# Kernel optimization log

Measured on AMD Instinct MI355X. Metric: run time of the kernel, lower is better.

## Reference

```python
import jax, jax.numpy as jnp
import numpy as np

B, C_IN, C_OUT, A, H, W = 32, 256, 512, 256, 64, 64


def setup_inputs() -> dict:
    key = jax.random.key(0)
    ks = jax.random.split(key, 8)
    s = 0.02
    return {
        "x": jax.random.normal(ks[0], (B, C_IN, H, W), dtype=jnp.float32),
        "g": jax.random.normal(ks[1], (B, C_OUT), dtype=jnp.float32),
        "Wg": jax.random.normal(ks[2], (A, C_OUT), dtype=jnp.float32) * s,
        "bg": jnp.full((A,), 0.1, dtype=jnp.float32),
        "Wx": jax.random.normal(ks[3], (A, C_IN), dtype=jnp.float32) * s,
        "bx": jnp.full((A,), 0.1, dtype=jnp.float32),
        "Wf": jax.random.normal(ks[4], (1, A), dtype=jnp.float32) * s,
        "bf": jnp.full((1,), 0.1, dtype=jnp.float32),
    }


def reference(x, g, Wg, bg, Wx, bx, Wf, bf):
    b, c, h, w = x.shape
    gg = g @ Wg.T + bg                                  # [B, A]
    xf = x.reshape(b, c, h * w)                          # [B, C, HW]
    # Linear_x applied per spatial position (batched instead of python loop)
    nx = jnp.einsum('bcn,ac->bna', xf, Wx) + bx          # [B, HW, A]
    nx = jax.nn.relu(gg[:, None, :] + nx)                # [B, HW, A]
    att = jnp.einsum('bna,a->bn', nx, Wf[0]) + bf[0]     # [B, HW]
    # min-subtract, sum-divide normalization
    att = att - jnp.min(att, axis=1, keepdims=True)
    att = att / jnp.sum(att, axis=1, keepdims=True)
    out = jnp.einsum('bcn,bn->bc', xf, att)              # weighted pooling [B, C]
    return out, att.reshape(b, h, w)
```

## Files before the change

### kernel.cpp

```cpp
#include <hip/hip_runtime.h>
#include <stdint.h>

#define B_   32
#define CIN  256
#define COUT 512
#define HW_  4096
#define NT   64

typedef short  short8  __attribute__((ext_vector_type(8)));
typedef float  float4_ __attribute__((ext_vector_type(4)));

__device__ __forceinline__ unsigned f2bf(float f) {
    unsigned u = __float_as_uint(f);
    u += 0x7FFFu + ((u >> 16) & 1u);
    return u >> 16;
}

__global__ __launch_bounds__(256) void prep_kernel(
    const float* __restrict__ g, const float* __restrict__ Wg,
    const float* __restrict__ bg, const float* __restrict__ Wx,
    const float* __restrict__ bx,
    uint4* __restrict__ WxR, float* __restrict__ ggbx,
    float* __restrict__ P, float* __restrict__ T)
{
    int t = threadIdx.x;
    if (blockIdx.x >= 32) {
        int e = (blockIdx.x - 32) * 256 + t;
        int lane = e & 63, ai = (e >> 6) & 3, kk = (e >> 8) & 7, w = e >> 11;
        int a  = w * 64 + ai * 16 + (lane & 15);
        int kb = kk * 32 + (lane >> 4) * 8;
        const float4* s = (const float4*)(Wx + (size_t)a * 256 + kb);
        float4 u0 = s[0], u1 = s[1];
        uint4 pk;
        pk.x = f2bf(u0.x) | (f2bf(u0.y) << 16);
        pk.y = f2bf(u0.z) | (f2bf(u0.w) << 16);
        pk.z = f2bf(u1.x) | (f2bf(u1.y) << 16);
        pk.w = f2bf(u1.z) | (f2bf(u1.w) << 16);
        WxR[e] = pk;
        return;
    }
    int b = blockIdx.x;
    int i = b * 256 + t;
    P[i] = 0.f; T[i] = 0.f;

    __shared__ float gl[COUT];
    gl[t]       = g[b * COUT + t];
    gl[t + 256] = g[b * COUT + 256 + t];
    __syncthreads();

    float acc0 = bg[t] + bx[t], acc1 = 0.f;
    const float4* wr = (const float4*)(Wg + (size_t)t * COUT);
    #pragma unroll 8
    for (int co = 0; co < COUT / 4; co += 2) {
        float4 wv0 = wr[co],     gv0 = *(const float4*)&gl[co * 4];
        float4 wv1 = wr[co + 1], gv1 = *(const float4*)&gl[co * 4 + 4];
        acc0 += wv0.x * gv0.x + wv0.y * gv0.y + wv0.z * gv0.z + wv0.w * gv0.w;
        acc1 += wv1.x * gv1.x + wv1.y * gv1.y + wv1.z * gv1.z + wv1.w * gv1.w;
    }
    ggbx[b * 256 + t] = acc0 + acc1;
}

__global__ __launch_bounds__(256, 2) void attn_main(
    const float* __restrict__ x, const char* __restrict__ WxR,
    const float* __restrict__ ggbx, const float* __restrict__ Wf,
    const float* __restrict__ bfs,
    float* __restrict__ P, float* __restrict__ T, float* __restrict__ raw)
{
    __shared__ float xTf[CIN * NT];
    __shared__ float att_part[4][NT];
    __shared__ float raw_l[NT];

    int bid = blockIdx.x;
    int b = bid >> 6, nt = bid & 63;
    int t = threadIdx.x, w = t >> 6, lane = t & 63;
    int quad = lane >> 4, l15 = lane & 15;

    const float* xb = x + (size_t)b * CIN * HW_ + nt * NT;

    {
        const float* gl0 = xb + (size_t)(lane >> 4) * HW_ + (lane & 15) * 4;
        #pragma unroll
        for (int j = 0; j < 16; j++) {
            int c0 = w * 64 + j * 4;
            __builtin_amdgcn_global_load_lds(
                (const __attribute__((address_space(1))) unsigned int*)(gl0 + (size_t)c0 * HW_),
                (__attribute__((address_space(3))) unsigned int*)&xTf[c0 * 64],
                16, 0, 0);
        }
    }

    float ga[4], wfv[4];
    #pragma unroll
    for (int ai = 0; ai < 4; ai++) {
        int a = w * 64 + ai * 16 + l15;
        ga[ai]  = ggbx[b * 256 + a];
        wfv[ai] = Wf[a];
    }

    float4_ acc[4][4];
    #pragma unroll
    for (int mi = 0; mi < 4; mi++)
        #pragma unroll
        for (int ai = 0; ai < 4; ai++)
            acc[mi][ai] = (float4_){0.f, 0.f, 0.f, 0.f};

    __syncthreads();

    const char* wsl = WxR + w * 32768 + lane * 16;
    short8 afA[4], bfA[4], afB[4], bfB[4];

    auto LDB = [&](short8* bf, int k0) {
        const char* wk = wsl + (k0 >> 5) * 4096;
        #pragma unroll
        for (int ai = 0; ai < 4; ai++)
            bf[ai] = *(const short8*)(wk + ai * 1024);
    };
    auto LDA = [&](short8* af, int k0) {
        int cb = k0 + quad * 8;
        #pragma unroll
        for (int mi = 0; mi < 4; mi++) {
            const float* bse = &xTf[cb * 64 + mi * 16 + l15];
            union { unsigned u[4]; short8 s; } cv;
            #pragma unroll
            for (int p = 0; p < 4; p++) {
                float f0 = bse[(2 * p) * 64];
                float f1 = bse[(2 * p + 1) * 64];
                cv.u[p] = f2bf(f0) | (f2bf(f1) << 16);
            }
            af[mi] = cv.s;
        }
    };
    auto MM = [&](short8* af, short8* bf) {
        #pragma unroll
        for (int mi = 0; mi < 4; mi++)
            #pragma unroll
            for (int ai = 0; ai < 4; ai++)
                acc[mi][ai] = __builtin_amdgcn_mfma_f32_16x16x32_bf16(
                    af[mi], bf[ai], acc[mi][ai], 0, 0, 0);
    };

    LDA(afA, 0);   LDB(bfA, 0);
    LDA(afB, 32);  LDB(bfB, 32);
    MM(afA, bfA);  LDA(afA, 64);  LDB(bfA, 64);
    MM(afB, bfB);  LDA(afB, 96);  LDB(bfB, 96);
    MM(afA, bfA);  LDA(afA, 128); LDB(bfA, 128);
    MM(afB, bfB);  LDA(afB, 160); LDB(bfB, 160);
    MM(afA, bfA);  LDA(afA, 192); LDB(bfA, 192);
    MM(afB, bfB);  LDA(afB, 224); LDB(bfB, 224);
    MM(afA, bfA);
    MM(afB, bfB);

    #pragma unroll
    for (int mi = 0; mi < 4; mi++) {
        float p[4] = {0.f, 0.f, 0.f, 0.f};
        #pragma unroll
        for (int ai = 0; ai < 4; ai++) {
            #pragma unroll
            for (int r = 0; r < 4; r++) {
                float vv = acc[mi][ai][r] + ga[ai];
                vv = fmaxf(vv, 0.f);
                p[r] = fmaf(vv, wfv[ai], p[r]);
            }
        }
        #pragma unroll
        for (int r = 0; r < 4; r++) {
            #pragma unroll
            for (int off = 1; off < 16; off <<= 1)
                p[r] += __shfl_xor(p[r], off, 16);
        }
        if (l15 == 0) {
            #pragma unroll
            for (int r = 0; r < 4; r++)
                att_part[w][mi * 16 + quad * 4 + r] = p[r];
        }
    }
    __syncthreads();

    if (t < NT) {
        float rv = att_part[0][t] + att_part[1][t] + att_part[2][t] + att_part[3][t] + bfs[0];
        raw[b * HW_ + nt * NT + t] = rv;
        raw_l[t] = rv;
    }
    __syncthreads();

    {
        float4_ rl = *(const float4_*)&raw_l[l15 * 4];
        #pragma unroll
        for (int ci = 0; ci < 16; ci++) {
            int c = w * 64 + ci * 4 + quad;
            float4_ xv = *(const float4_*)&xTf[c * 64 + l15 * 4];
            float pp = xv[0] * rl[0] + xv[1] * rl[1] + xv[2] * rl[2] + xv[3] * rl[3];
            float tt = (xv[0] + xv[1]) + (xv[2] + xv[3]);
            #pragma unroll
            for (int off = 1; off < 16; off <<= 1) {
                pp += __shfl_xor(pp, off, 16);
                tt += __shfl_xor(tt, off, 16);
            }
            if (l15 == 0) {
                atomicAdd(&P[b * 256 + c], pp);
                atomicAdd(&T[b * 256 + c], tt);
            }
        }
    }
}

__global__ __launch_bounds__(256) void finalize_kernel(
    const float* __restrict__ raw, const float* __restrict__ P,
    const float* __restrict__ T, float* __restrict__ out)
{
    int b = blockIdx.x, t = threadIdx.x;
    const float* r = raw + (size_t)b * HW_;
    float v[16];
    float mn = 3.4e38f, sm = 0.f;
    #pragma unroll
    for (int i = 0; i < 16; i++) {
        v[i] = r[t + 256 * i];
        mn = fminf(mn, v[i]);
        sm += v[i];
    }
    #pragma unroll
    for (int off = 1; off < 64; off <<= 1) {
        mn = fminf(mn, __shfl_xor(mn, off, 64));
        sm += __shfl_xor(sm, off, 64);
    }
    __shared__ float smn[4], ssm[4];
    int w = t >> 6;
    if ((t & 63) == 0) { smn[w] = mn; ssm[w] = sm; }
    __syncthreads();
    mn = fminf(fminf(smn[0], smn[1]), fminf(smn[2], smn[3]));
    sm = (ssm[0] + ssm[1]) + (ssm[2] + ssm[3]);
    float S = sm - 4096.f * mn;
    float inv = 1.f / S;

    float* att = out + B_ * CIN + (size_t)b * HW_;
    #pragma unroll
    for (int i = 0; i < 16; i++) att[t + 256 * i] = (v[i] - mn) * inv;

    int ic = b * 256 + t;
    out[ic] = (P[ic] - mn * T[ic]) * inv;
}

extern "C" void kernel_launch(void* const* d_in, const int* in_sizes, int n_in,
                              void* d_out, int out_size, void* d_ws, size_t ws_size,
                              hipStream_t stream)
{
    const float* x   = (const float*)d_in[0];
    const float* g   = (const float*)d_in[1];
    const float* Wg  = (const float*)d_in[2];
    const float* bg  = (const float*)d_in[3];
    const float* Wx  = (const float*)d_in[4];
    const float* bx  = (const float*)d_in[5];
    const float* Wf  = (const float*)d_in[6];
    const float* bf  = (const float*)d_in[7];
    float* out = (float*)d_out;

    char* wsb = (char*)d_ws;
    uint4* WxR  = (uint4*)wsb;
    float* ggbx = (float*)(wsb + 131072);
    float* P    = ggbx + 8192;
    float* T    = P + 8192;
    float* raw  = T + 8192;

    prep_kernel<<<64, 256, 0, stream>>>(g, Wg, bg, Wx, bx, WxR, ggbx, P, T);
    attn_main<<<2048, 256, 0, stream>>>(x, (const char*)WxR, ggbx, Wf, bf, P, T, raw);
    finalize_kernel<<<32, 256, 0, stream>>>(raw, P, T, out);
}
```

Measured before the change: 277.5 us.

## Make attention blocks persistent over 8 tiles with bf16 swizzled LDS and register prefetch

Each block now handles 8 consecutive 32-position tiles instead of one 64-position tile, so the grid shrinks from 2048 to 512 blocks. The x tile for the next step is prefetched into registers while the current tile computes, then converted once to bf16 and written to a swizzled, transposed LDS layout. This halves LDS use, removes the repeated per-MFMA float-to-bf16 conversion, and lets three blocks share a CU. The pooled sums stay in per-thread registers and are written with a single atomic per channel instead of per-tile atomics. The cost is that the pooling sums are now computed from bf16-rounded x, which may reduce accuracy, and per-tile barriers add serialization within each block.

New measurement: 373.7 us. 34.7% more time.

```diff
diff --git a/kernel.cpp b/kernel.cpp
--- a/kernel.cpp
+++ b/kernel.cpp
@@ -5,7 +5,8 @@
 #define CIN  256
 #define COUT 512
 #define HW_  4096
-#define NT   64
+#define NT   32
+#define TPB  8
 
 typedef short  short8  __attribute__((ext_vector_type(8)));
 typedef float  float4_ __attribute__((ext_vector_type(4)));
@@ -14,6 +15,9 @@
     unsigned u = __float_as_uint(f);
     u += 0x7FFFu + ((u >> 16) & 1u);
     return u >> 16;
+}
+__device__ __forceinline__ float bf2f(unsigned h) {
+    return __uint_as_float(h << 16);
 }
 
 __global__ __launch_bounds__(256) void prep_kernel(
@@ -60,34 +64,27 @@
     ggbx[b * 256 + t] = acc0 + acc1;
 }
 
-__global__ __launch_bounds__(256, 2) void attn_main(
+__global__ __launch_bounds__(256, 3) void attn_main(
     const float* __restrict__ x, const char* __restrict__ WxR,
     const float* __restrict__ ggbx, const float* __restrict__ Wf,
     const float* __restrict__ bfs,
     float* __restrict__ P, float* __restrict__ T, float* __restrict__ raw)
 {
-    __shared__ float xTf[CIN * NT];
+    __shared__ unsigned int xT[NT * 128];
     __shared__ float att_part[4][NT];
     __shared__ float raw_l[NT];
 
-    int bid = blockIdx.x;
-    int b = bid >> 6, nt = bid & 63;
+    int bl = blockIdx.x;
+    int b   = bl >> 4;
+    int nt0 = (bl & 15) * TPB;
     int t = threadIdx.x, w = t >> 6, lane = t & 63;
     int quad = lane >> 4, l15 = lane & 15;
 
-    const float* xb = x + (size_t)b * CIN * HW_ + nt * NT;
-
-    {
-        const float* gl0 = xb + (size_t)(lane >> 4) * HW_ + (lane & 15) * 4;
-        #pragma unroll
-        for (int j = 0; j < 16; j++) {
-            int c0 = w * 64 + j * 4;
-            __builtin_amdgcn_global_load_lds(
-                (const __attribute__((address_space(1))) unsigned int*)(gl0 + (size_t)c0 * HW_),
-                (__attribute__((address_space(3))) unsigned int*)&xTf[c0 * 64],
-                16, 0, 0);
-        }
-    }
+    const float* xb = x + (size_t)b * CIN * HW_;
+
+    int sub = lane >> 3, n4 = (lane & 7) * 4;
+    int cbase = w * 64 + sub * 8;
+    int ch = cbase >> 3;
 
     float ga[4], wfv[4];
     #pragma unroll
@@ -96,112 +93,136 @@
         ga[ai]  = ggbx[b * 256 + a];
         wfv[ai] = Wf[a];
     }
-
-    float4_ acc[4][4];
-    #pragma unroll
-    for (int mi = 0; mi < 4; mi++)
-        #pragma unroll
-        for (int ai = 0; ai < 4; ai++)
-            acc[mi][ai] = (float4_){0.f, 0.f, 0.f, 0.f};
-
+    float bfv = bfs[0];
+
+    const char* wsl = WxR + w * 32768 + lane * 16;
+
+    float pp_tot = 0.f, tt_tot = 0.f;
+
+    float4_ v[8];
+    auto LOADX = [&](int nt) {
+        const float* p0 = xb + (size_t)cbase * HW_ + nt * NT + n4;
+        #pragma unroll
+        for (int j = 0; j < 8; j++)
+            v[j] = *(const float4_*)(p0 + (size_t)j * HW_);
+    };
+    auto STAGE = [&]() {
+        #pragma unroll
+        for (int r = 0; r < 4; r++) {
+            uint4 pk;
+            pk.x = f2bf(v[0][r]) | (f2bf(v[1][r]) << 16);
+            pk.y = f2bf(v[2][r]) | (f2bf(v[3][r]) << 16);
+            pk.z = f2bf(v[4][r]) | (f2bf(v[5][r]) << 16);
+            pk.w = f2bf(v[6][r]) | (f2bf(v[7][r]) << 16);
+            int n = n4 + r;
+            int p = (ch ^ n ^ (n >> 3)) & 31;
+            *(uint4*)&xT[n * 128 + p * 4] = pk;
+        }
+    };
+
+    LOADX(nt0);
+    STAGE();
     __syncthreads();
 
-    const char* wsl = WxR + w * 32768 + lane * 16;
-    short8 afA[4], bfA[4], afB[4], bfB[4];
-
-    auto LDB = [&](short8* bf, int k0) {
-        const char* wk = wsl + (k0 >> 5) * 4096;
-        #pragma unroll
-        for (int ai = 0; ai < 4; ai++)
-            bf[ai] = *(const short8*)(wk + ai * 1024);
-    };
-    auto LDA = [&](short8* af, int k0) {
-        int cb = k0 + quad * 8;
-        #pragma unroll
-        for (int mi = 0; mi < 4; mi++) {
-            const float* bse = &xTf[cb * 64 + mi * 16 + l15];
-            union { unsigned u[4]; short8 s; } cv;
-            #pragma unroll
-            for (int p = 0; p < 4; p++) {
-                float f0 = bse[(2 * p) * 64];
-                float f1 = bse[(2 * p + 1) * 64];
-                cv.u[p] = f2bf(f0) | (f2bf(f1) << 16);
-            }
-            af[mi] = cv.s;
-        }
-    };
-    auto MM = [&](short8* af, short8* bf) {
-        #pragma unroll
-        for (int mi = 0; mi < 4; mi++)
+    for (int i = 0; i < TPB; i++) {
+        int nt = nt0 + i;
+        if (i < TPB - 1) LOADX(nt + 1);
+
+        float4_ acc[2][4];
+        #pragma unroll
+        for (int mi = 0; mi < 2; mi++)
             #pragma unroll
             for (int ai = 0; ai < 4; ai++)
-                acc[mi][ai] = __builtin_amdgcn_mfma_f32_16x16x32_bf16(
-                    af[mi], bf[ai], acc[mi][ai], 0, 0, 0);
-    };
-
-    LDA(afA, 0);   LDB(bfA, 0);
-    LDA(afB, 32);  LDB(bfB, 32);
-    MM(afA, bfA);  LDA(afA, 64);  LDB(bfA, 64);
-    MM(afB, bfB);  LDA(afB, 96);  LDB(bfB, 96);
-    MM(afA, bfA);  LDA(afA, 128); LDB(bfA, 128);
-    MM(afB, bfB);  LDA(afB, 160); LDB(bfB, 160);
-    MM(afA, bfA);  LDA(afA, 192); LDB(bfA, 192);
-    MM(afB, bfB);  LDA(afB, 224); LDB(bfB, 224);
-    MM(afA, bfA);
-    MM(afB, bfB);
-
-    #pragma unroll
-    for (int mi = 0; mi < 4; mi++) {
-        float p[4] = {0.f, 0.f, 0.f, 0.f};
-        #pragma unroll
-        for (int ai = 0; ai < 4; ai++) {
+                acc[mi][ai] = (float4_){0.f, 0.f, 0.f, 0.f};
+
+        short8 af[2], bfA[4], bfB[4];
+        auto LDA = [&](int k0) {
+            int qk = (k0 >> 3) + quad;
+            #pragma unroll
+            for (int mi = 0; mi < 2; mi++) {
+                int n = mi * 16 + l15;
+                int p = (qk ^ n ^ (n >> 3)) & 31;
+                af[mi] = *(const short8*)&xT[n * 128 + p * 4];
+            }
+        };
+        auto LDB = [&](short8* bf, int k0) {
+            const char* wk = wsl + (k0 >> 5) * 4096;
+            #pragma unroll
+            for (int ai = 0; ai < 4; ai++)
+                bf[ai] = *(const short8*)(wk + ai * 1024);
+        };
+        auto MM = [&](short8* bf) {
+            #pragma unroll
+            for (int mi = 0; mi < 2; mi++)
+                #pragma unroll
+                for (int ai = 0; ai < 4; ai++)
+                    acc[mi][ai] = __builtin_amdgcn_mfma_f32_16x16x32_bf16(
+                        af[mi], bf[ai], acc[mi][ai], 0, 0, 0);
+        };
+
+        LDB(bfA, 0);
+        LDB(bfB, 32);
+        #pragma unroll
+        for (int k0 = 0; k0 < 256; k0 += 64) {
+            LDA(k0);      MM(bfA);  if (k0 < 192) LDB(bfA, k0 + 64);
+            LDA(k0 + 32); MM(bfB);  if (k0 < 192) LDB(bfB, k0 + 96);
+        }
+
+        #pragma unroll
+        for (int mi = 0; mi < 2; mi++) {
+            float p[4] = {0.f, 0.f, 0.f, 0.f};
+            #pragma unroll
+            for (int ai = 0; ai < 4; ai++) {
+                #pragma unroll
+                for (int r = 0; r < 4; r++) {
+                    float vv = acc[mi][ai][r] + ga[ai];
+                    vv = fmaxf(vv, 0.f);
+                    p[r] = fmaf(vv, wfv[ai], p[r]);
+                }
+            }
             #pragma unroll
             for (int r = 0; r < 4; r++) {
-                float vv = acc[mi][ai][r] + ga[ai];
-                vv = fmaxf(vv, 0.f);
-                p[r] = fmaf(vv, wfv[ai], p[r]);
-            }
-        }
-        #pragma unroll
-        for (int r = 0; r < 4; r++) {
-            #pragma unroll
-            for (int off = 1; off < 16; off <<= 1)
-                p[r] += __shfl_xor(p[r], off, 16);
-        }
-        if (l15 == 0) {
-            #pragma unroll
-            for (int r = 0; r < 4; r++)
-                att_part[w][mi * 16 + quad * 4 + r] = p[r];
-        }
-    }
-    __syncthreads();
-
-    if (t < NT) {
-        float rv = att_part[0][t] + att_part[1][t] + att_part[2][t] + att_part[3][t] + bfs[0];
-        raw[b * HW_ + nt * NT + t] = rv;
-        raw_l[t] = rv;
-    }
-    __syncthreads();
-
-    {
-        float4_ rl = *(const float4_*)&raw_l[l15 * 4];
-        #pragma unroll
-        for (int ci = 0; ci < 16; ci++) {
-            int c = w * 64 + ci * 4 + quad;
-            float4_ xv = *(const float4_*)&xTf[c * 64 + l15 * 4];
-            float pp = xv[0] * rl[0] + xv[1] * rl[1] + xv[2] * rl[2] + xv[3] * rl[3];
-            float tt = (xv[0] + xv[1]) + (xv[2] + xv[3]);
-            #pragma unroll
-            for (int off = 1; off < 16; off <<= 1) {
-                pp += __shfl_xor(pp, off, 16);
-                tt += __shfl_xor(tt, off, 16);
+                #pragma unroll
+                for (int off = 1; off < 16; off <<= 1)
+                    p[r] += __shfl_xor(p[r], off, 16);
             }
             if (l15 == 0) {
-                atomicAdd(&P[b * 256 + c], pp);
-                atomicAdd(&T[b * 256 + c], tt);
-            }
-        }
-    }
+                #pragma unroll
+                for (int r = 0; r < 4; r++)
+                    att_part[w][mi * 16 + quad * 4 + r] = p[r];
+            }
+        }
+        __syncthreads();
+
+        if (t < NT) {
+            float rv = att_part[0][t] + att_part[1][t] + att_part[2][t]
+                     + att_part[3][t] + bfv;
+            raw[b * HW_ + nt * NT + t] = rv;
+            raw_l[t] = rv;
+        }
+        __syncthreads();
+
+        {
+            int chp = t >> 3, qw = (t >> 1) & 3, hi = t & 1;
+            #pragma unroll
+            for (int n = 0; n < NT; n++) {
+                int p = (chp ^ n ^ (n >> 3)) & 31;
+                unsigned u = xT[n * 128 + p * 4 + qw];
+                float xv = bf2f(hi ? (u >> 16) : (u & 0xFFFFu));
+                pp_tot = fmaf(xv, raw_l[n], pp_tot);
+                tt_tot += xv;
+            }
+        }
+        __syncthreads();
+
+        if (i < TPB - 1) {
+            STAGE();
+            __syncthreads();
+        }
+    }
+
+    atomicAdd(&P[b * 256 + t], pp_tot);
+    atomicAdd(&T[b * 256 + t], tt_tot);
 }
 
 __global__ __launch_bounds__(256) void finalize_kernel(
@@ -262,6 +283,6 @@
     float* raw  = T + 8192;
 
     prep_kernel<<<64, 256, 0, stream>>>(g, Wg, bg, Wx, bx, WxR, ggbx, P, T);
-    attn_main<<<2048, 256, 0, stream>>>(x, (const char*)WxR, ggbx, Wf, bf, P, T, raw);
+    attn_main<<<512, 256, 0, stream>>>(x, (const char*)WxR, ggbx, Wf, bf, P, T, raw);
     finalize_kernel<<<32, 256, 0, stream>>>(raw, P, T, out);
 }
```
